# Kernel optimization log

Hardware: AMD Instinct MI355X
Metric: run time of the kernel (lower is better)

## Reference

```python
import jax, jax.numpy as jnp
import numpy as np

B, C, H, W = 8, 256, 128, 128
HEADS = 8


def setup_inputs() -> dict:
    key = jax.random.key(0)
    ks = jax.random.split(key, 9)
    d = {"x": jax.random.normal(ks[0], (B, C, H, W), jnp.float32)}
    for i, name in enumerate(["q", "k", "v", "o"]):
        # 1x1 conv == dense over channel dim; weight [C_out, C_in]
        d["W" + name] = jax.random.normal(ks[1 + 2 * i], (C, C), jnp.float32) * (C ** -0.5)
        d["b" + name] = jax.random.normal(ks[2 + 2 * i], (C,), jnp.float32) * 0.01
    return d


def reference(x, Wq, bq, Wk, bk, Wv, bv, Wo, bo):
    b, c, h, w = x.shape
    heads = HEADS
    hd = c // heads
    scale = hd ** -0.5

    def proj(Wm, bm):
        y = jnp.einsum('bchw,oc->bohw', x, Wm) + bm[None, :, None, None]
        return y.reshape(b, heads, hd, h, w)

    q = proj(Wq, bq)
    k = proj(Wk, bk)
    v = proj(Wv, bv)

    # horizontal attention: per row y, attention over width positions (w x v)
    attn_h = jax.nn.softmax(jnp.einsum('bhdyw,bhdyv->bhywv', q, k) * scale, axis=-1)
    out_h = jnp.einsum('bhywv,bhdyv->bhdyw', attn_h, v)

    # vertical attention: per column w, attention over height positions (y x z)
    attn_w = jax.nn.softmax(jnp.einsum('bhdyw,bhdzw->bhwyz', q, k) * scale, axis=-1)
    out_w = jnp.einsum('bhwyz,bhdzw->bhdyw', attn_w, v)

    out = (out_h + out_w).reshape(b, c, h, w)
    out = jnp.einsum('bchw,oc->bohw', out, Wo) + bo[None, :, None, None]
    return out + x
```

## Files before the change

kernel.cpp:

```cpp
#include <hip/hip_runtime.h>

#define B_ 8
#define C_ 256
#define HH 128
#define WW 128
#define HEADS_ 8
#define SCALE 0.17677669529663687f

typedef short v8s __attribute__((ext_vector_type(8)));
typedef float f32x4 __attribute__((ext_vector_type(4)));

__device__ __forceinline__ unsigned short f2bf(float f){
  unsigned int u = __float_as_uint(f);
  u += 0x7FFFu + ((u>>16)&1u);
  return (unsigned short)(u>>16);
}
__device__ __forceinline__ float bf2f(unsigned short s){ return __uint_as_float(((unsigned int)s)<<16); }
__device__ __forceinline__ f32x4 mfma16(v8s a, v8s b, f32x4 c){
  return __builtin_amdgcn_mfma_f32_16x16x32_bf16(a,b,c,0,0,0);
}
__device__ __forceinline__ int xs_idx(int s,int c){ return s*256 + ((((c>>3)^(s&31))&31)<<3) + (c&7); }
__device__ __forceinline__ int wl_idx(int dm,int c){ return dm*256 + ((((c>>3)^(dm&31))&31)<<3) + (c&7); }
__device__ __forceinline__ void gload_lds16(const void* g, void* l){
  __builtin_amdgcn_global_load_lds((const __attribute__((address_space(1))) unsigned int*)g,
                                   (__attribute__((address_space(3))) unsigned int*)l, 16, 0, 0);
}

#define WS_OFF_AH 201850880ULL

__global__ __launch_bounds__(512,4)
void prep_w_kernel(const float* __restrict__ Wq, const float* __restrict__ Wk,
                   const float* __restrict__ Wv, const float* __restrict__ Wo,
                   unsigned short* __restrict__ wsW, unsigned short* __restrict__ wsWo){
  const int bid = blockIdx.x, t = threadIdx.x;
  if (bid < 96){
    int h = bid/12, seg = bid%12;
    int dm = seg*8 + (t>>6), c = (t&63)*4;
    const float* Wm = dm<32 ? Wq : (dm<64 ? Wk : Wv);
    const float4 w4 = *(const float4*)&Wm[(h*32 + (dm&31))*C_ + c];
    ushort4 pk = { f2bf(w4.x), f2bf(w4.y), f2bf(w4.z), f2bf(w4.w) };
    *(ushort4*)(wsW + h*24576 + wl_idx(dm, c)) = pk;
  } else {
    int q = bid - 96;
    int oc = q>>2, seg = q&3;
    int o = seg*8 + (t>>6), c = (t&63)*4;
    const float4 w4 = *(const float4*)&Wo[(oc*32+o)*C_ + c];
    ushort4 pk = { f2bf(w4.x), f2bf(w4.y), f2bf(w4.z), f2bf(w4.w) };
    *(ushort4*)(wsWo + oc*8192 + wl_idx(o, c)) = pk;
  }
}

__global__ __launch_bounds__(512,4)
void proj3_kernel(const float* __restrict__ x,
                  const float* __restrict__ bq, const float* __restrict__ bk,
                  const float* __restrict__ bv,
                  const unsigned short* __restrict__ wsW,
                  unsigned short* __restrict__ Qw, unsigned short* __restrict__ Kw,
                  unsigned short* __restrict__ Vw){
  __shared__ __align__(16) char smem[76800];
  unsigned short* xs = (unsigned short*)smem;
  unsigned short* wl = (unsigned short*)smem;
  unsigned short* rp = (unsigned short*)(smem + 49152);
  float* biasl       = (float*)(smem + 75776);

  const int tid = threadIdx.x;
  const int b = blockIdx.x >> 7, pt = blockIdx.x & 127;
  const size_t pos0 = (size_t)pt * 128;

  {
    const int cq = (tid>>5)*2, pl = (tid&31)*4;
    #pragma unroll
    for (int j=0;j<8;++j){
      int c0 = j*32 + cq;
      const float4 a0 = *(const float4*)&x[((size_t)(b*C_ + c0  ))*16384 + pos0 + pl];
      const float4 a1 = *(const float4*)&x[((size_t)(b*C_ + c0+1))*16384 + pos0 + pl];
      unsigned int p0 = (unsigned)f2bf(a0.x) | ((unsigned)f2bf(a1.x)<<16);
      unsigned int p1 = (unsigned)f2bf(a0.y) | ((unsigned)f2bf(a1.y)<<16);
      unsigned int p2 = (unsigned)f2bf(a0.z) | ((unsigned)f2bf(a1.z)<<16);
      unsigned int p3 = (unsigned)f2bf(a0.w) | ((unsigned)f2bf(a1.w)<<16);
      *(unsigned int*)&xs[xs_idx(pl+0, c0)] = p0;
      *(unsigned int*)&xs[xs_idx(pl+1, c0)] = p1;
      *(unsigned int*)&xs[xs_idx(pl+2, c0)] = p2;
      *(unsigned int*)&xs[xs_idx(pl+3, c0)] = p3;
    }
  }
  __syncthreads();

  const int lane = tid&63, wv = tid>>6, lr = lane&15, lk = lane>>4;
  v8s areg[8];
  #pragma unroll
  for (int ks=0;ks<8;++ks) areg[ks] = *(const v8s*)(xs + xs_idx(wv*16+lr, ks*32+lk*8));
  __syncthreads();

  {
    const char* wb = (const char*)wsW;
    for (int rIt=0;rIt<6;++rIt)
      gload_lds16(wb + (rIt*512+tid)*16, (char*)wl + (rIt*512+tid)*16);
  }

  const f32x4 zero4 = {0.f,0.f,0.f,0.f};
  for (int h=0; h<HEADS_; ++h){
    __syncthreads();
    if (tid<96){
      int mat = tid>>5;
      const float* bm = mat==0?bq:(mat==1?bk:bv);
      biasl[tid] = bm[h*32 + (tid&31)];
    }
    f32x4 acc[6];
    #pragma unroll
    for (int n=0;n<6;++n) acc[n]=zero4;
    #pragma unroll
    for (int ks=0;ks<8;++ks){
      int c0 = ks*32 + lk*8;
      #pragma unroll
      for (int n=0;n<6;++n){
        v8s bb = *(const v8s*)(wl + wl_idx(n*16+lr, c0));
        acc[n] = mfma16(areg[ks], bb, acc[n]);
      }
    }
    __syncthreads();
    if (h < HEADS_-1){
      const char* wb = (const char*)wsW + (h+1)*49152;
      for (int rIt=0;rIt<6;++rIt)
        gload_lds16(wb + (rIt*512+tid)*16, (char*)wl + (rIt*512+tid)*16);
    }
    #pragma unroll
    for (int n=0;n<6;++n){
      int dm = n*16+lr;
      float bia = biasl[dm];
      #pragma unroll
      for (int rr=0;rr<4;++rr){
        int pos = wv*16 + lk*4 + rr;
        float val = acc[n][rr] + bia;
        if (n<2) val *= SCALE;
        rp[pos*104 + dm] = f2bf(val);
      }
    }
    __syncthreads();
    {
      int p = tid>>2, ch = tid&3;
      v8s qd = *(const v8s*)&rp[p*104 +      ch*8];
      v8s kd = *(const v8s*)&rp[p*104 + 32 + ch*8];
      v8s vd = *(const v8s*)&rp[p*104 + 64 + ch*8];
      size_t og = ((size_t)(b*HEADS_+h)*16384 + pos0 + p)*32 + ch*8;
      *(v8s*)(Qw + og) = qd;
      *(v8s*)(Kw + og) = kd;
      *(v8s*)(Vw + og) = vd;
    }
  }
}

template<int VERT>
__global__ __launch_bounds__(512,6)
void attn2_kernel(const unsigned short* __restrict__ Qw, const unsigned short* __restrict__ Kw,
                  const unsigned short* __restrict__ Vw, unsigned short* __restrict__ Ah){
  __shared__ __align__(16) char smem[37376];
  unsigned short* kl = (unsigned short*)smem;
  unsigned short* Vt = (unsigned short*)(smem + 10240);
  float*          ob = (float*)(smem + 18944);

  const int tid = threadIdx.x;
  int b, head, fix;
  if (VERT){ int xcd = blockIdx.x&7, rest = blockIdx.x>>3;
             fix = xcd*16 + (rest&15); head = (rest>>4)&7; b = rest>>7; }
  else     { head = blockIdx.x&7; fix = (blockIdx.x>>3)&127; b = blockIdx.x>>10; }
  const size_t tb = (size_t)(b*HEADS_+head)*16384*32;
  const int lane = tid&63, wvq = tid>>6, lr = lane&15, lk = lane>>4;
  const f32x4 zero4 = {0.f,0.f,0.f,0.f};

  {
    int pl = tid>>2, ch = tid&3;
    size_t g = tb + (VERT ? ((size_t)pl*128 + fix) : ((size_t)fix*128 + pl))*32 + ch*8;
    v8s kv = *(const v8s*)(Kw + g);
    v8s vv = *(const v8s*)(Vw + g);
    *(v8s*)&kl[pl*40 + ch*8] = kv;
    int slot = (pl & ~31) | (((pl>>2)&3)<<3) | (((pl>>4)&1)<<2) | (pl&3);
    #pragma unroll
    for (int j=0;j<8;++j) Vt[(ch*8+j)*136 + slot] = (unsigned short)vv[j];
  }
  const int posq = VERT ? (wvq*16+lr)*128 + fix : fix*128 + (wvq*16+lr);
  v8s qa = *(const v8s*)(Qw + tb + (size_t)posq*32 + lk*8);
  __syncthreads();

  f32x4 sc[8];
  #pragma unroll
  for (int kt=0;kt<8;++kt){
    v8s kb = *(const v8s*)&kl[(kt*16+lr)*40 + lk*8];
    sc[kt] = mfma16(kb, qa, zero4);
  }
  float mx = sc[0][0];
  #pragma unroll
  for (int kt=0;kt<8;++kt){
    #pragma unroll
    for (int rr=0;rr<4;++rr) mx = fmaxf(mx, sc[kt][rr]);
  }
  mx = fmaxf(mx, __shfl_xor(mx, 16));
  mx = fmaxf(mx, __shfl_xor(mx, 32));
  float sm = 0.f;
  #pragma unroll
  for (int kt=0;kt<8;++kt){
    #pragma unroll
    for (int rr=0;rr<4;++rr){ float p = __expf(sc[kt][rr]-mx); sc[kt][rr]=p; sm += p; }
  }
  sm += __shfl_xor(sm, 16);
  sm += __shfl_xor(sm, 32);
  const float rn = 1.f/sm;
  unsigned int pk[16];
  #pragma unroll
  for (int kt=0;kt<8;++kt){
    pk[kt*2  ] = (unsigned)f2bf(sc[kt][0]*rn) | ((unsigned)f2bf(sc[kt][1]*rn)<<16);
    pk[kt*2+1] = (unsigned)f2bf(sc[kt][2]*rn) | ((unsigned)f2bf(sc[kt][3]*rn)<<16);
  }
  f32x4 o0 = zero4, o1 = zero4;
  #pragma unroll
  for (int ks=0;ks<4;++ks){
    union { unsigned int u[4]; v8s v; } pa;
    pa.u[0]=pk[4*ks]; pa.u[1]=pk[4*ks+1]; pa.u[2]=pk[4*ks+2]; pa.u[3]=pk[4*ks+3];
    v8s v0 = *(const v8s*)&Vt[(     lr)*136 + ks*32 + lk*8];
    v8s v1 = *(const v8s*)&Vt[(16 + lr)*136 + ks*32 + lk*8];
    o0 = mfma16(pa.v, v0, o0);
    o1 = mfma16(pa.v, v1, o1);
  }
  #pragma unroll
  for (int rr=0;rr<4;++rr){
    int s = wvq*16 + lk*4 + rr;
    ob[s*36 + lr     ] = o0[rr];
    ob[s*36 + 16 + lr] = o1[rr];
  }
  {
    int row = wvq*16 + (lane>>2), jj = lane&3;
    f32x4 fa = *(const f32x4*)&ob[row*36 + jj*8];
    f32x4 fb = *(const f32x4*)&ob[row*36 + jj*8 + 4];
    int pos = VERT ? row*128 + fix : fix*128 + row;
    size_t ga = ((size_t)b*16384 + pos)*256 + (size_t)(((head*4+jj)^(pos&31))<<3);
    if (VERT){
      v8s prev = *(const v8s*)(Ah + ga);
      v8s outv;
      #pragma unroll
      for (int j=0;j<4;++j){
        outv[j]   = (short)f2bf(bf2f((unsigned short)prev[j])   + fa[j]);
        outv[4+j] = (short)f2bf(bf2f((unsigned short)prev[4+j]) + fb[j]);
      }
      *(v8s*)(Ah + ga) = outv;
    } else {
      v8s outv;
      #pragma unroll
      for (int j=0;j<4;++j){
        outv[j]   = (short)f2bf(fa[j]);
        outv[4+j] = (short)f2bf(fb[j]);
      }
      *(v8s*)(Ah + ga) = outv;
    }
  }
}

__global__ __launch_bounds__(512,1)
void final2_kernel(const float* __restrict__ x, const unsigned short* __restrict__ wsWo,
                   const float* __restrict__ bo, const unsigned short* __restrict__ Ah,
                   float* __restrict__ out)
{
  __shared__ __align__(16) char smem[82048];
  unsigned short* asl = (unsigned short*)smem;
  unsigned short* wol = (unsigned short*)(smem + 65536);
  float* bol          = (float*)(smem + 81920);

  const int tid = threadIdx.x;
  const int b = blockIdx.x >> 7, pt = blockIdx.x & 127;
  {
    const char* ab = (const char*)(Ah + ((size_t)b*16384 + (size_t)pt*128)*256);
    for (int i=0;i<8;++i)
      gload_lds16(ab + (i*512+tid)*16, (char*)asl + (i*512+tid)*16);
  }
  const int lane = tid & 63, wv = tid >> 6;
  const int lr = lane & 15, lk = lane >> 4;
  const f32x4 zero4 = {0.f,0.f,0.f,0.f};

  for (int oc = 0; oc < 8; ++oc){
    {
      const char* wb = (const char*)wsWo + oc*16384;
      for (int rIt=0;rIt<2;++rIt)
        gload_lds16(wb + (rIt*512+tid)*16, (char*)wol + (rIt*512+tid)*16);
    }
    if (tid < 32) bol[tid] = bo[oc*32 + tid];
    __syncthreads();

    f32x4 a0 = zero4, a1 = zero4;
    #pragma unroll
    for (int ks = 0; ks < 8; ++ks){
      int c0 = ks*32 + lk*8;
      v8s av = *(const v8s*)(asl + xs_idx(wv*16 + lr, c0));
      v8s b0 = *(const v8s*)(wol + wl_idx(     lr, c0));
      v8s b1 = *(const v8s*)(wol + wl_idx(16 + lr, c0));
      a0 = mfma16(av, b0, a0);
      a1 = mfma16(av, b1, a1);
    }
    {
      int base0 = ((b*C_ + oc*32 + lr)*HH)*WW + pt*128 + wv*16 + lk*4;
      f32x4 xv0 = *(const f32x4*)(x + base0);
      f32x4 xv1 = *(const f32x4*)(x + base0 + 16*HH*WW);
      f32x4 r0 = a0 + xv0 + bol[lr];
      f32x4 r1 = a1 + xv1 + bol[16 + lr];
      *(f32x4*)(out + base0) = r0;
      *(f32x4*)(out + base0 + 16*HH*WW) = r1;
    }
    __syncthreads();
  }
}

extern "C" void kernel_launch(void* const* d_in, const int* in_sizes, int n_in,
                              void* d_out, int out_size, void* d_ws, size_t ws_size,
                              hipStream_t stream) {
  const float* x  = (const float*)d_in[0];
  const float* Wq = (const float*)d_in[1];
  const float* bq = (const float*)d_in[2];
  const float* Wk = (const float*)d_in[3];
  const float* bk = (const float*)d_in[4];
  const float* Wv = (const float*)d_in[5];
  const float* bv = (const float*)d_in[6];
  const float* Wo = (const float*)d_in[7];
  const float* bo = (const float*)d_in[8];
  float* out = (float*)d_out;

  unsigned short* wsW  = (unsigned short*)d_ws;
  unsigned short* wsWo = (unsigned short*)((char*)d_ws + 393216);
  unsigned short* Qw   = (unsigned short*)((char*)d_ws + 524288);
  unsigned short* Kw   = Qw + 33554432;
  unsigned short* Vw   = Kw + 33554432;
  unsigned short* Ah   = (unsigned short*)((char*)d_ws + WS_OFF_AH);

  prep_w_kernel<<<dim3(128),  dim3(512), 0, stream>>>(Wq, Wk, Wv, Wo, wsW, wsWo);
  proj3_kernel <<<dim3(1024), dim3(512), 0, stream>>>(x, bq, bk, bv, wsW, Qw, Kw, Vw);
  attn2_kernel<0><<<dim3(8192), dim3(512), 0, stream>>>(Qw, Kw, Vw, Ah);
  attn2_kernel<1><<<dim3(8192), dim3(512), 0, stream>>>(Qw, Kw, Vw, Ah);
  final2_kernel<<<dim3(1024), dim3(512), 0, stream>>>(x, wsWo, bo, Ah, out);
}
```

Measured before the change: 282.2 us.

## Retile QKV projection waves 2x3, defer head writeback, drop bias LDS

After: 316.1 us. +12.0%, slower.

```diff
diff --git a/kernel.cpp b/kernel.cpp
--- a/kernel.cpp
+++ b/kernel.cpp
@@ -51,7 +51,7 @@
 }
 
 __global__ __launch_bounds__(512,4)
-void proj3_kernel(const float* __restrict__ x,
+void proj4_kernel(const float* __restrict__ x,
                   const float* __restrict__ bq, const float* __restrict__ bk,
                   const float* __restrict__ bv,
                   const unsigned short* __restrict__ wsW,
@@ -61,7 +61,6 @@
   unsigned short* xs = (unsigned short*)smem;
   unsigned short* wl = (unsigned short*)smem;
   unsigned short* rp = (unsigned short*)(smem + 49152);
-  float* biasl       = (float*)(smem + 75776);
 
   const int tid = threadIdx.x;
   const int b = blockIdx.x >> 7, pt = blockIdx.x & 127;
@@ -87,9 +86,14 @@
   __syncthreads();
 
   const int lane = tid&63, wv = tid>>6, lr = lane&15, lk = lane>>4;
-  v8s areg[8];
-  #pragma unroll
-  for (int ks=0;ks<8;++ks) areg[ks] = *(const v8s*)(xs + xs_idx(wv*16+lr, ks*32+lk*8));
+  const int mbase = (wv&3)*2;
+  const int nb    = (wv>>2)*3;
+  v8s areg0[8], areg1[8];
+  #pragma unroll
+  for (int ks=0;ks<8;++ks){
+    areg0[ks] = *(const v8s*)(xs + xs_idx((mbase  )*16+lr, ks*32+lk*8));
+    areg1[ks] = *(const v8s*)(xs + xs_idx((mbase+1)*16+lr, ks*32+lk*8));
+  }
   __syncthreads();
 
   {
@@ -99,23 +103,37 @@
   }
 
   const f32x4 zero4 = {0.f,0.f,0.f,0.f};
+  const int wp = tid>>2, wch = tid&3;
+
   for (int h=0; h<HEADS_; ++h){
     __syncthreads();
-    if (tid<96){
-      int mat = tid>>5;
-      const float* bm = mat==0?bq:(mat==1?bk:bv);
-      biasl[tid] = bm[h*32 + (tid&31)];
-    }
-    f32x4 acc[6];
-    #pragma unroll
-    for (int n=0;n<6;++n) acc[n]=zero4;
+    float bias_[3];
+    #pragma unroll
+    for (int ni=0;ni<3;++ni){
+      int n = nb + ni;
+      const float* bm = (n>>1)==0 ? bq : ((n>>1)==1 ? bk : bv);
+      bias_[ni] = bm[h*32 + (n&1)*16 + lr];
+    }
+    if (h > 0){
+      v8s qd = *(const v8s*)&rp[wp*104 +      wch*8];
+      v8s kd = *(const v8s*)&rp[wp*104 + 32 + wch*8];
+      v8s vd = *(const v8s*)&rp[wp*104 + 64 + wch*8];
+      size_t og = ((size_t)(b*HEADS_+(h-1))*16384 + pos0 + wp)*32 + wch*8;
+      *(v8s*)(Qw + og) = qd;
+      *(v8s*)(Kw + og) = kd;
+      *(v8s*)(Vw + og) = vd;
+    }
+    f32x4 acc[3][2];
+    #pragma unroll
+    for (int ni=0;ni<3;++ni){ acc[ni][0]=zero4; acc[ni][1]=zero4; }
     #pragma unroll
     for (int ks=0;ks<8;++ks){
       int c0 = ks*32 + lk*8;
       #pragma unroll
-      for (int n=0;n<6;++n){
-        v8s bb = *(const v8s*)(wl + wl_idx(n*16+lr, c0));
-        acc[n] = mfma16(areg[ks], bb, acc[n]);
+      for (int ni=0;ni<3;++ni){
+        v8s bb = *(const v8s*)(wl + wl_idx((nb+ni)*16+lr, c0));
+        acc[ni][0] = mfma16(areg0[ks], bb, acc[ni][0]);
+        acc[ni][1] = mfma16(areg1[ks], bb, acc[ni][1]);
       }
     }
     __syncthreads();
@@ -125,28 +143,31 @@
         gload_lds16(wb + (rIt*512+tid)*16, (char*)wl + (rIt*512+tid)*16);
     }
     #pragma unroll
-    for (int n=0;n<6;++n){
-      int dm = n*16+lr;
-      float bia = biasl[dm];
+    for (int ni=0;ni<3;++ni){
+      int n = nb + ni;
+      int dm = n*16 + lr;
+      float bia = bias_[ni];
       #pragma unroll
-      for (int rr=0;rr<4;++rr){
-        int pos = wv*16 + lk*4 + rr;
-        float val = acc[n][rr] + bia;
-        if (n<2) val *= SCALE;
-        rp[pos*104 + dm] = f2bf(val);
+      for (int mi=0;mi<2;++mi){
+        #pragma unroll
+        for (int rr=0;rr<4;++rr){
+          int pos = (mbase+mi)*16 + lk*4 + rr;
+          float val = acc[ni][mi][rr] + bia;
+          if (n<2) val *= SCALE;
+          rp[pos*104 + dm] = f2bf(val);
+        }
       }
     }
-    __syncthreads();
-    {
-      int p = tid>>2, ch = tid&3;
-      v8s qd = *(const v8s*)&rp[p*104 +      ch*8];
-      v8s kd = *(const v8s*)&rp[p*104 + 32 + ch*8];
-      v8s vd = *(const v8s*)&rp[p*104 + 64 + ch*8];
-      size_t og = ((size_t)(b*HEADS_+h)*16384 + pos0 + p)*32 + ch*8;
-      *(v8s*)(Qw + og) = qd;
-      *(v8s*)(Kw + og) = kd;
-      *(v8s*)(Vw + og) = vd;
-    }
+  }
+  __syncthreads();
+  {
+    v8s qd = *(const v8s*)&rp[wp*104 +      wch*8];
+    v8s kd = *(const v8s*)&rp[wp*104 + 32 + wch*8];
+    v8s vd = *(const v8s*)&rp[wp*104 + 64 + wch*8];
+    size_t og = ((size_t)(b*HEADS_+7)*16384 + pos0 + wp)*32 + wch*8;
+    *(v8s*)(Qw + og) = qd;
+    *(v8s*)(Kw + og) = kd;
+    *(v8s*)(Vw + og) = vd;
   }
 }
 
@@ -254,15 +275,14 @@
   }
 }
 
-__global__ __launch_bounds__(512,1)
+__global__ __launch_bounds__(512,4)
 void final2_kernel(const float* __restrict__ x, const unsigned short* __restrict__ wsWo,
                    const float* __restrict__ bo, const unsigned short* __restrict__ Ah,
                    float* __restrict__ out)
 {
-  __shared__ __align__(16) char smem[82048];
+  __shared__ __align__(16) char smem[81920];
   unsigned short* asl = (unsigned short*)smem;
   unsigned short* wol = (unsigned short*)(smem + 65536);
-  float* bol          = (float*)(smem + 81920);
 
   const int tid = threadIdx.x;
   const int b = blockIdx.x >> 7, pt = blockIdx.x & 127;
@@ -281,7 +301,7 @@
       for (int rIt=0;rIt<2;++rIt)
         gload_lds16(wb + (rIt*512+tid)*16, (char*)wol + (rIt*512+tid)*16);
     }
-    if (tid < 32) bol[tid] = bo[oc*32 + tid];
+    const float b0v = bo[oc*32 + lr], b1v = bo[oc*32 + 16 + lr];
     __syncthreads();
 
     f32x4 a0 = zero4, a1 = zero4;
@@ -298,8 +318,8 @@
       int base0 = ((b*C_ + oc*32 + lr)*HH)*WW + pt*128 + wv*16 + lk*4;
       f32x4 xv0 = *(const f32x4*)(x + base0);
       f32x4 xv1 = *(const f32x4*)(x + base0 + 16*HH*WW);
-      f32x4 r0 = a0 + xv0 + bol[lr];
-      f32x4 r1 = a1 + xv1 + bol[16 + lr];
+      f32x4 r0 = a0 + xv0 + b0v;
+      f32x4 r1 = a1 + xv1 + b1v;
       *(f32x4*)(out + base0) = r0;
       *(f32x4*)(out + base0 + 16*HH*WW) = r1;
     }
@@ -329,7 +349,7 @@
   unsigned short* Ah   = (unsigned short*)((char*)d_ws + WS_OFF_AH);
 
   prep_w_kernel<<<dim3(128),  dim3(512), 0, stream>>>(Wq, Wk, Wv, Wo, wsW, wsWo);
-  proj3_kernel <<<dim3(1024), dim3(512), 0, stream>>>(x, bq, bk, bv, wsW, Qw, Kw, Vw);
+  proj4_kernel <<<dim3(1024), dim3(512), 0, stream>>>(x, bq, bk, bv, wsW, Qw, Kw, Vw);
   attn2_kernel<0><<<dim3(8192), dim3(512), 0, stream>>>(Qw, Kw, Vw, Ah);
   attn2_kernel<1><<<dim3(8192), dim3(512), 0, stream>>>(Qw, Kw, Vw, Ah);
   final2_kernel<<<dim3(1024), dim3(512), 0, stream>>>(x, wsWo, bo, Ah, out);
```
